# Performance work log

Measured on AMD Instinct MI355X. Metric: run time of the kernel, lower is better.

## Reference

```python
import jax, jax.numpy as jnp
import numpy as np

NUM_FIELDS = 40
EMBED_DIM = 64
IN_SUB = 40
OUT_SUB = 40
BATCH = 256


def setup_inputs() -> dict:
    key = jax.random.key(0)
    k0, k1 = jax.random.split(key)
    B0 = jax.random.normal(k0, (BATCH, NUM_FIELDS, EMBED_DIM), dtype=jnp.float32)
    Bi = jax.random.normal(k1, (BATCH, IN_SUB, EMBED_DIM), dtype=jnp.float32)
    # parameters, initialized exactly as in the torch module
    W = jnp.tile(jnp.eye(EMBED_DIM, dtype=jnp.float32)[None], (OUT_SUB, 1, 1))  # (n, D, D)
    alpha = jnp.ones((NUM_FIELDS, IN_SUB, OUT_SUB), dtype=jnp.float32)          # (f, i, n)
    h = jnp.ones((OUT_SUB, EMBED_DIM, 1), dtype=jnp.float32)                    # (n, D, 1)
    return {"B0": B0, "Bi": Bi, "W": W, "alpha": alpha, "h": h}


def reference(B0, Bi, W, alpha, h):
    # Math of the original: fusion[b,n,D,d] = sum_{f,i} B0[b,f,D]*Bi[b,i,d]*alpha[f,i,n]
    # (equivalent to the 5D outer product contracted with alpha, but never
    #  materializes the (b,f,i,D,D) tensor).
    fusion = jnp.einsum('bfD,bid,fin->bnDd', B0, Bi, alpha)  # (b, n, D, D)
    # elementwise scale by W then project with h: out[b,n,D] = sum_d fusion*W*h
    out = jnp.einsum('bnDd,nDd,nd->bnD', fusion, W, h[..., 0])
    return out
```

## Files before the change

kernel.cpp:

```cpp
#include <hip/hip_runtime.h>
#include <hip/hip_bf16.h>

#define NF 40
#define NI 40
#define NN 40
#define ED 64
#define NB 256

typedef __attribute__((ext_vector_type(8))) short   short8;
typedef __attribute__((ext_vector_type(8))) __bf16  bf16x8;
typedef __attribute__((ext_vector_type(4))) float   f32x4;

__device__ __forceinline__ unsigned short f2bf(float x) {
    union { float f; unsigned u; } v; v.f = x;
    unsigned r = v.u + 0x7FFFu + ((v.u >> 16) & 1u);
    return (unsigned short)(r >> 16);
}

__device__ __forceinline__ bf16x8 ld_frag(const unsigned short* p) {
    return __builtin_bit_cast(bf16x8, *(const short8*)p);
}

__device__ __forceinline__ f32x4 mfma16(bf16x8 a, bf16x8 b, f32x4 c) {
    return __builtin_amdgcn_mfma_f32_16x16x32_bf16(a, b, c, 0, 0, 0);
}

#define WHP_N (64 * 64)
#define ALP_N (48 * 64)
#define BFT_N 7168
#define BI_OFF 0
#define B0T_OFF (48 * 64)
#define BPB 2

__global__ __launch_bounds__(256) void gif_prep5(
        const float* __restrict__ B0, const float* __restrict__ Bi,
        const float* __restrict__ W, const float* __restrict__ alpha,
        const float* __restrict__ h,
        unsigned short* __restrict__ whp, unsigned short* __restrict__ alp,
        unsigned short* __restrict__ bft) {
    const int x = blockIdx.x;
    const int t = threadIdx.x;
    if (x < NN) {
        const int n = x;
        for (int idx = t; idx < 64 * 64; idx += 256) {
            int d = idx & 63;
            whp[n * WHP_N + idx] = f2bf(W[n * ED * ED + idx] * h[n * ED + d]);
        }
        for (int idx = t; idx < 8 * 64; idx += 256)
            alp[n * ALP_N + (40 + (idx >> 6)) * 64 + (idx & 63)] = 0;
        for (int idx = t; idx < 40 * 24; idx += 256) {
            int i = idx / 24, f = 40 + idx - i * 24;
            alp[n * ALP_N + i * 64 + f] = 0;
        }
    } else if (x < NN + NF) {
        const int f = x - NN;
        for (int idx = t; idx < NI * NN; idx += 256) {
            int i = idx / NN, n = idx - i * NN;
            alp[n * ALP_N + i * 64 + f] = f2bf(alpha[(f * NI + i) * NN + n]);
        }
    } else {
        const int b = x - (NN + NF);
        unsigned short* dst = bft + (size_t)b * BFT_N;
        __shared__ __align__(16) unsigned short sT[64 * 72];

        const float4* biv = (const float4*)(Bi + (size_t)b * NI * ED);
        const float4* b0v = (const float4*)(B0 + (size_t)b * NF * ED);
        float4 rb[3], r0[3];
#pragma unroll
        for (int k = 0; k < 3; ++k) {
            const int c = t + k * 256;
            if (c < 640) { rb[k] = biv[c]; r0[k] = b0v[c]; }
        }

        for (int idx = t; idx < 64 * 32; idx += 256)
            sT[(idx >> 5) * 72 + 40 + (idx & 31)] = 0;

#pragma unroll
        for (int k = 0; k < 3; ++k) {
            const int c = t + k * 256;
            if (c < 640) {
                const int i = c >> 4, d0 = (c & 15) * 4;
                ushort4 pk;
                pk.x = f2bf(rb[k].x); pk.y = f2bf(rb[k].y);
                pk.z = f2bf(rb[k].z); pk.w = f2bf(rb[k].w);
                const int chunk = (d0 >> 3) ^ (i & 7);
                *(ushort4*)&dst[BI_OFF + i * 64 + (chunk << 3) + (d0 & 7)] = pk;
            }
        }
        for (int idx = t; idx < 8 * 64; idx += 256)
            dst[BI_OFF + (40 + (idx >> 6)) * 64 + (idx & 63)] = 0;

#pragma unroll
        for (int k = 0; k < 3; ++k) {
            const int c = t + k * 256;
            if (c < 640) {
                const int f = c >> 4, D0 = (c & 15) * 4;
                sT[(D0 + 0) * 72 + f] = f2bf(r0[k].x);
                sT[(D0 + 1) * 72 + f] = f2bf(r0[k].y);
                sT[(D0 + 2) * 72 + f] = f2bf(r0[k].z);
                sT[(D0 + 3) * 72 + f] = f2bf(r0[k].w);
            }
        }
        __syncthreads();

        for (int g = t; g < 512; g += 256) {
            const int D = g >> 3, pc = g & 7;
            short8 v = *(const short8*)&sT[D * 72 + ((pc ^ (D & 7)) << 3)];
            *(short8*)&dst[B0T_OFF + D * 64 + (pc << 3)] = v;
        }
    }
}

__global__ __launch_bounds__(256, 2) void gif_main9(
        const unsigned short* __restrict__ whp,
        const unsigned short* __restrict__ alp,
        const unsigned short* __restrict__ bft,
        float* __restrict__ out) {
    const int bg = blockIdx.x;
    const int ng = blockIdx.y;
    const int t = threadIdx.x;
    const int lane = t & 63, w = t >> 6;
    const int quad = lane >> 4, l15 = lane & 15, fo = quad * 8;
    const int n = ng * 4 + w;

    __shared__ __align__(16) unsigned short sBuf[2 * BFT_N];

    const short8* src = (const short8*)(bft + (size_t)(bg * BPB) * BFT_N);
    short8 st[7];
#pragma unroll
    for (int k = 0; k < 7; ++k) st[k] = src[t + k * 256];

    bf16x8 alA[3][2], whB[4][2];
    {
        const unsigned short* ap = alp + n * ALP_N;
        const unsigned short* wp = whp + n * WHP_N;
#pragma unroll
        for (int m = 0; m < 3; ++m)
#pragma unroll
            for (int s = 0; s < 2; ++s)
                alA[m][s] = ld_frag(&ap[(m * 16 + l15) * 64 + s * 32 + fo]);
#pragma unroll
        for (int tt = 0; tt < 4; ++tt)
#pragma unroll
            for (int s = 0; s < 2; ++s)
                whB[tt][s] = ld_frag(&wp[(tt * 16 + l15) * 64 + s * 32 + fo]);
    }

#pragma unroll
    for (int k = 0; k < 7; ++k)
        *(short8*)&sBuf[(size_t)(t + k * 256) * 8] = st[k];
    __syncthreads();

#pragma unroll
    for (int j = 0; j < BPB; ++j) {
        const unsigned short* sb = &sBuf[j * BFT_N];
        const int b = bg * BPB + j;

        bf16x8 biA[3][2];
#pragma unroll
        for (int m = 0; m < 3; ++m)
#pragma unroll
            for (int s = 0; s < 2; ++s) {
                const int row = m * 16 + l15;
                const int pch = ((s * 4 + quad) ^ (row & 7)) << 3;
                biA[m][s] = ld_frag(&sb[BI_OFF + row * 64 + pch]);
            }

        float p[4];
#pragma unroll
        for (int tt = 0; tt < 4; ++tt) {
            const int row = tt * 16 + l15;
            const int pc0 = ((0 + quad) ^ (row & 7)) << 3;
            const int pc1 = ((4 + quad) ^ (row & 7)) << 3;
            bf16x8 bb0 = ld_frag(&sb[B0T_OFF + row * 64 + pc0]);
            bf16x8 bb1 = ld_frag(&sb[B0T_OFF + row * 64 + pc1]);
            float acc = 0.f;
#pragma unroll
            for (int m = 0; m < 3; ++m) {
                f32x4 z = {0.f, 0.f, 0.f, 0.f};
                f32x4 T = mfma16(biA[m][0], whB[tt][0], z);
                T = mfma16(biA[m][1], whB[tt][1], T);
                f32x4 G = mfma16(alA[m][0], bb0, z);
                G = mfma16(alA[m][1], bb1, G);
                acc += T[0] * G[0] + T[1] * G[1] + T[2] * G[2] + T[3] * G[3];
            }
            p[tt] = acc;
        }
#pragma unroll
        for (int tt = 0; tt < 4; ++tt) {
            p[tt] += __shfl_xor(p[tt], 16, 64);
            p[tt] += __shfl_xor(p[tt], 32, 64);
        }
        float v = (quad == 0) ? p[0] : (quad == 1) ? p[1] : (quad == 2) ? p[2] : p[3];
        out[((size_t)b * NN + n) * ED + lane] = v;
    }
}

#define PS 72

__device__ __forceinline__ bf16x8 mk_al_frag(const float* __restrict__ alpha,
        int n, int m, int s, int l15, int quad) {
    bf16x8 r;
    const int row = m * 16 + l15;
    const int f0 = s * 32 + quad * 8;
#pragma unroll
    for (int j = 0; j < 8; ++j) {
        const int f = f0 + j;
        float v = (row < NI && f < NF) ? alpha[(f * NI + row) * NN + n] : 0.f;
        r[j] = (__bf16)v;
    }
    return r;
}
__device__ __forceinline__ bf16x8 mk_wh_frag(const float* __restrict__ W,
        const float* __restrict__ h, int n, int tt, int s, int l15, int quad) {
    bf16x8 r;
    const int row = tt * 16 + l15;
    const int k0 = s * 32 + quad * 8;
#pragma unroll
    for (int j = 0; j < 8; ++j) {
        float v = W[n * ED * ED + row * ED + k0 + j] * h[n * ED + k0 + j];
        r[j] = (__bf16)v;
    }
    return r;
}

__global__ __launch_bounds__(256) void gif_mfma(
        const float* __restrict__ B0, const float* __restrict__ Bi,
        const float* __restrict__ W, const float* __restrict__ alpha,
        const float* __restrict__ h, float* __restrict__ out) {
    const int q = blockIdx.x >> 8;
    const int b = blockIdx.x & 255;

    __shared__ __align__(16) unsigned short sBi[48 * PS];
    __shared__ __align__(16) unsigned short sBT[ED * PS];

    const int t = threadIdx.x;
    for (int idx = t; idx < 48 * PS; idx += 256) {
        int i = idx / PS, c = idx - i * PS;
        sBi[idx] = (i < NI && c < ED) ? f2bf(Bi[b * NI * ED + i * ED + c])
                                      : (unsigned short)0;
    }
    for (int idx = t; idx < ED * PS; idx += 256) {
        int D = idx / PS, c = idx - D * PS;
        sBT[idx] = (c < NF) ? f2bf(B0[b * NF * ED + c * ED + D])
                            : (unsigned short)0;
    }
    __syncthreads();

    const int lane = t & 63, w = t >> 6;
    const int quad = lane >> 4, l15 = lane & 15;
    const int fragoff = quad * 8;

    bf16x8 biA[3][2], b0B[4][2];
#pragma unroll
    for (int m = 0; m < 3; ++m)
#pragma unroll
        for (int s = 0; s < 2; ++s)
            biA[m][s] = ld_frag(&sBi[(m * 16 + l15) * PS + s * 32 + fragoff]);
#pragma unroll
    for (int tt = 0; tt < 4; ++tt)
#pragma unroll
        for (int s = 0; s < 2; ++s)
            b0B[tt][s] = ld_frag(&sBT[(tt * 16 + l15) * PS + s * 32 + fragoff]);

#pragma unroll
    for (int rep = 0; rep < 2; ++rep) {
        const int n = q * 8 + w + rep * 4;

        bf16x8 alA[3][2];
#pragma unroll
        for (int m = 0; m < 3; ++m)
#pragma unroll
            for (int s = 0; s < 2; ++s)
                alA[m][s] = mk_al_frag(alpha, n, m, s, l15, quad);

        float p[4];
#pragma unroll
        for (int tt = 0; tt < 4; ++tt) {
            bf16x8 whB2[2];
            whB2[0] = mk_wh_frag(W, h, n, tt, 0, l15, quad);
            whB2[1] = mk_wh_frag(W, h, n, tt, 1, l15, quad);
            float acc = 0.f;
#pragma unroll
            for (int m = 0; m < 3; ++m) {
                f32x4 z = {0.f, 0.f, 0.f, 0.f};
                f32x4 T = mfma16(biA[m][0], whB2[0], z);
                T = mfma16(biA[m][1], whB2[1], T);
                f32x4 G = mfma16(alA[m][0], b0B[tt][0], z);
                G = mfma16(alA[m][1], b0B[tt][1], G);
                acc += T[0] * G[0] + T[1] * G[1] + T[2] * G[2] + T[3] * G[3];
            }
            p[tt] = acc;
        }
#pragma unroll
        for (int tt = 0; tt < 4; ++tt) {
            p[tt] += __shfl_xor(p[tt], 16, 64);
            p[tt] += __shfl_xor(p[tt], 32, 64);
        }
        float v = (quad == 0) ? p[0] : (quad == 1) ? p[1] : (quad == 2) ? p[2] : p[3];
        out[(b * NN + n) * ED + lane] = v;
    }
}

extern "C" void kernel_launch(void* const* d_in, const int* in_sizes, int n_in,
                              void* d_out, int out_size, void* d_ws, size_t ws_size,
                              hipStream_t stream) {
    const float* B0    = (const float*)d_in[0];
    const float* Bi    = (const float*)d_in[1];
    const float* W     = (const float*)d_in[2];
    const float* alpha = (const float*)d_in[3];
    const float* h     = (const float*)d_in[4];
    float* out = (float*)d_out;

    const size_t need = (size_t)(NN * WHP_N + NN * ALP_N + NB * BFT_N)
                        * sizeof(unsigned short);
    if (ws_size >= need) {
        unsigned short* whp = (unsigned short*)d_ws;
        unsigned short* alp = whp + (size_t)NN * WHP_N;
        unsigned short* bft = alp + (size_t)NN * ALP_N;
        gif_prep5<<<NN + NF + NB, 256, 0, stream>>>(B0, Bi, W, alpha, h,
                                                    whp, alp, bft);
        gif_main9<<<dim3(NB / BPB, 10), 256, 0, stream>>>(whp, alp, bft, out);
        return;
    }

    gif_mfma<<<5 * NB, 256, 0, stream>>>(B0, Bi, W, alpha, h, out);
}
```

Before: 79.86 us.

## Fuse per-batch B0/Bi bf16 conversion into main kernel, one block per batch

The per-batch fp32-to-bf16 conversion and B0 transpose move from the prep kernel into the main kernel. That kernel now runs one 512-thread block per batch item and loops over all 40 output subspaces across 8 waves. This removes the workspace round-trip for the converted batch tiles and lets each block reuse its Bi/B0T fragments across all n. In exchange, alpha and W*h fragments are reloaded from global memory per n inside the loop. The grid shrinks to 256 blocks, which may lower parallelism.

New measurement: 85.16 us. 6.6% more time.

```diff
diff --git a/kernel.cpp b/kernel.cpp
--- a/kernel.cpp
+++ b/kernel.cpp
@@ -27,17 +27,11 @@
 
 #define WHP_N (64 * 64)
 #define ALP_N (48 * 64)
-#define BFT_N 7168
-#define BI_OFF 0
-#define B0T_OFF (48 * 64)
-#define BPB 2
-
-__global__ __launch_bounds__(256) void gif_prep5(
-        const float* __restrict__ B0, const float* __restrict__ Bi,
+
+__global__ __launch_bounds__(256) void gif_prep4(
         const float* __restrict__ W, const float* __restrict__ alpha,
         const float* __restrict__ h,
-        unsigned short* __restrict__ whp, unsigned short* __restrict__ alp,
-        unsigned short* __restrict__ bft) {
+        unsigned short* __restrict__ whp, unsigned short* __restrict__ alp) {
     const int x = blockIdx.x;
     const int t = threadIdx.x;
     if (x < NN) {
@@ -52,88 +46,95 @@
             int i = idx / 24, f = 40 + idx - i * 24;
             alp[n * ALP_N + i * 64 + f] = 0;
         }
-    } else if (x < NN + NF) {
+    } else {
         const int f = x - NN;
         for (int idx = t; idx < NI * NN; idx += 256) {
             int i = idx / NN, n = idx - i * NN;
             alp[n * ALP_N + i * 64 + f] = f2bf(alpha[(f * NI + i) * NN + n]);
         }
-    } else {
-        const int b = x - (NN + NF);
-        unsigned short* dst = bft + (size_t)b * BFT_N;
-        __shared__ __align__(16) unsigned short sT[64 * 72];
-
-        const float4* biv = (const float4*)(Bi + (size_t)b * NI * ED);
-        const float4* b0v = (const float4*)(B0 + (size_t)b * NF * ED);
-        float4 rb[3], r0[3];
-#pragma unroll
-        for (int k = 0; k < 3; ++k) {
-            const int c = t + k * 256;
-            if (c < 640) { rb[k] = biv[c]; r0[k] = b0v[c]; }
-        }
-
-        for (int idx = t; idx < 64 * 32; idx += 256)
-            sT[(idx >> 5) * 72 + 40 + (idx & 31)] = 0;
-
-#pragma unroll
-        for (int k = 0; k < 3; ++k) {
-            const int c = t + k * 256;
-            if (c < 640) {
-                const int i = c >> 4, d0 = (c & 15) * 4;
-                ushort4 pk;
-                pk.x = f2bf(rb[k].x); pk.y = f2bf(rb[k].y);
-                pk.z = f2bf(rb[k].z); pk.w = f2bf(rb[k].w);
-                const int chunk = (d0 >> 3) ^ (i & 7);
-                *(ushort4*)&dst[BI_OFF + i * 64 + (chunk << 3) + (d0 & 7)] = pk;
-            }
-        }
-        for (int idx = t; idx < 8 * 64; idx += 256)
-            dst[BI_OFF + (40 + (idx >> 6)) * 64 + (idx & 63)] = 0;
-
-#pragma unroll
-        for (int k = 0; k < 3; ++k) {
-            const int c = t + k * 256;
-            if (c < 640) {
-                const int f = c >> 4, D0 = (c & 15) * 4;
-                sT[(D0 + 0) * 72 + f] = f2bf(r0[k].x);
-                sT[(D0 + 1) * 72 + f] = f2bf(r0[k].y);
-                sT[(D0 + 2) * 72 + f] = f2bf(r0[k].z);
-                sT[(D0 + 3) * 72 + f] = f2bf(r0[k].w);
-            }
-        }
-        __syncthreads();
-
-        for (int g = t; g < 512; g += 256) {
-            const int D = g >> 3, pc = g & 7;
-            short8 v = *(const short8*)&sT[D * 72 + ((pc ^ (D & 7)) << 3)];
-            *(short8*)&dst[B0T_OFF + D * 64 + (pc << 3)] = v;
-        }
-    }
-}
-
-__global__ __launch_bounds__(256, 2) void gif_main9(
+    }
+}
+
+__global__ __launch_bounds__(512, 2) void gif_main10(
+        const float* __restrict__ B0, const float* __restrict__ Bi,
         const unsigned short* __restrict__ whp,
         const unsigned short* __restrict__ alp,
-        const unsigned short* __restrict__ bft,
         float* __restrict__ out) {
-    const int bg = blockIdx.x;
-    const int ng = blockIdx.y;
+    const int b = blockIdx.x;
     const int t = threadIdx.x;
     const int lane = t & 63, w = t >> 6;
     const int quad = lane >> 4, l15 = lane & 15, fo = quad * 8;
-    const int n = ng * 4 + w;
-
-    __shared__ __align__(16) unsigned short sBuf[2 * BFT_N];
-
-    const short8* src = (const short8*)(bft + (size_t)(bg * BPB) * BFT_N);
-    short8 st[7];
-#pragma unroll
-    for (int k = 0; k < 7; ++k) st[k] = src[t + k * 256];
-
-    bf16x8 alA[3][2], whB[4][2];
+
+    __shared__ __align__(16) unsigned short sBi[48 * 64];
+    __shared__ __align__(16) unsigned short sBT[64 * 64];
+
+    float4 rb[2], r0[2];
     {
-        const unsigned short* ap = alp + n * ALP_N;
-        const unsigned short* wp = whp + n * WHP_N;
+        const float4* biv = (const float4*)(Bi + (size_t)b * NI * ED);
+        const float4* b0v = (const float4*)(B0 + (size_t)b * NF * ED);
+#pragma unroll
+        for (int k = 0; k < 2; ++k) {
+            const int c = t + k * 512;
+            if (c < 640) { rb[k] = biv[c]; r0[k] = b0v[c]; }
+        }
+    }
+
+    for (int idx = t; idx < 8 * 64; idx += 512)
+        sBi[(40 + (idx >> 6)) * 64 + (idx & 63)] = 0;
+    for (int idx = t; idx < 64 * 24; idx += 512) {
+        const int D = idx / 24, rem = idx - D * 24;
+        const int c = 5 + (rem >> 3), j = rem & 7;
+        sBT[D * 64 + ((c ^ (D & 7)) << 3) + j] = 0;
+    }
+
+#pragma unroll
+    for (int k = 0; k < 2; ++k) {
+        const int c = t + k * 512;
+        if (c < 640) {
+            const int i = c >> 4, d0 = (c & 15) * 4;
+            ushort4 pk;
+            pk.x = f2bf(rb[k].x); pk.y = f2bf(rb[k].y);
+            pk.z = f2bf(rb[k].z); pk.w = f2bf(rb[k].w);
+            const int chunk = (d0 >> 3) ^ (i & 7);
+            *(ushort4*)&sBi[i * 64 + (chunk << 3) + (d0 & 7)] = pk;
+
+            const int f = c >> 4, D0 = (c & 15) * 4;
+            const float fv[4] = {r0[k].x, r0[k].y, r0[k].z, r0[k].w};
+#pragma unroll
+            for (int r = 0; r < 4; ++r) {
+                const int D = D0 + r;
+                const int ch = (f >> 3) ^ (D & 7);
+                sBT[D * 64 + (ch << 3) + (f & 7)] = f2bf(fv[r]);
+            }
+        }
+    }
+    __syncthreads();
+
+    bf16x8 biA[3][2], bb[4][2];
+#pragma unroll
+    for (int m = 0; m < 3; ++m)
+#pragma unroll
+        for (int s = 0; s < 2; ++s) {
+            const int row = m * 16 + l15;
+            const int pch = ((s * 4 + quad) ^ (row & 7)) << 3;
+            biA[m][s] = ld_frag(&sBi[row * 64 + pch]);
+        }
+#pragma unroll
+    for (int tt = 0; tt < 4; ++tt)
+#pragma unroll
+        for (int s = 0; s < 2; ++s) {
+            const int row = tt * 16 + l15;
+            const int pch = ((s * 4 + quad) ^ (row & 7)) << 3;
+            bb[tt][s] = ld_frag(&sBT[row * 64 + pch]);
+        }
+
+#pragma unroll
+    for (int k = 0; k < 5; ++k) {
+        const int n = k * 8 + w;
+        const unsigned short* ap = alp + (size_t)n * ALP_N;
+        const unsigned short* wp = whp + (size_t)n * WHP_N;
+
+        bf16x8 alA[3][2], whB[4][2];
 #pragma unroll
         for (int m = 0; m < 3; ++m)
 #pragma unroll
@@ -144,44 +145,18 @@
 #pragma unroll
             for (int s = 0; s < 2; ++s)
                 whB[tt][s] = ld_frag(&wp[(tt * 16 + l15) * 64 + s * 32 + fo]);
-    }
-
-#pragma unroll
-    for (int k = 0; k < 7; ++k)
-        *(short8*)&sBuf[(size_t)(t + k * 256) * 8] = st[k];
-    __syncthreads();
-
-#pragma unroll
-    for (int j = 0; j < BPB; ++j) {
-        const unsigned short* sb = &sBuf[j * BFT_N];
-        const int b = bg * BPB + j;
-
-        bf16x8 biA[3][2];
-#pragma unroll
-        for (int m = 0; m < 3; ++m)
-#pragma unroll
-            for (int s = 0; s < 2; ++s) {
-                const int row = m * 16 + l15;
-                const int pch = ((s * 4 + quad) ^ (row & 7)) << 3;
-                biA[m][s] = ld_frag(&sb[BI_OFF + row * 64 + pch]);
-            }
 
         float p[4];
 #pragma unroll
         for (int tt = 0; tt < 4; ++tt) {
-            const int row = tt * 16 + l15;
-            const int pc0 = ((0 + quad) ^ (row & 7)) << 3;
-            const int pc1 = ((4 + quad) ^ (row & 7)) << 3;
-            bf16x8 bb0 = ld_frag(&sb[B0T_OFF + row * 64 + pc0]);
-            bf16x8 bb1 = ld_frag(&sb[B0T_OFF + row * 64 + pc1]);
             float acc = 0.f;
 #pragma unroll
             for (int m = 0; m < 3; ++m) {
                 f32x4 z = {0.f, 0.f, 0.f, 0.f};
                 f32x4 T = mfma16(biA[m][0], whB[tt][0], z);
                 T = mfma16(biA[m][1], whB[tt][1], T);
-                f32x4 G = mfma16(alA[m][0], bb0, z);
-                G = mfma16(alA[m][1], bb1, G);
+                f32x4 G = mfma16(alA[m][0], bb[tt][0], z);
+                G = mfma16(alA[m][1], bb[tt][1], G);
                 acc += T[0] * G[0] + T[1] * G[1] + T[2] * G[2] + T[3] * G[3];
             }
             p[tt] = acc;
@@ -312,15 +287,12 @@
     const float* h     = (const float*)d_in[4];
     float* out = (float*)d_out;
 
-    const size_t need = (size_t)(NN * WHP_N + NN * ALP_N + NB * BFT_N)
-                        * sizeof(unsigned short);
+    const size_t need = (size_t)(NN * WHP_N + NN * ALP_N) * sizeof(unsigned short);
     if (ws_size >= need) {
         unsigned short* whp = (unsigned short*)d_ws;
         unsigned short* alp = whp + (size_t)NN * WHP_N;
-        unsigned short* bft = alp + (size_t)NN * ALP_N;
-        gif_prep5<<<NN + NF + NB, 256, 0, stream>>>(B0, Bi, W, alpha, h,
-                                                    whp, alp, bft);
-        gif_main9<<<dim3(NB / BPB, 10), 256, 0, stream>>>(whp, alp, bft, out);
+        gif_prep4<<<NN + NF, 256, 0, stream>>>(W, alpha, h, whp, alp);
+        gif_main10<<<NB, 512, 0, stream>>>(B0, Bi, whp, alp, out);
         return;
     }
 
```
